# Kernel tuning notes

Hardware: AMD Instinct MI355X
Metric: run time of the kernel (lower is better)

The kernel has to match this reference:

```python
import jax, jax.numpy as jnp
import numpy as np

B = 2
DIMS = ((41, 800, 800), (21, 400, 400), (11, 200, 200), (6, 100, 100))  # (D,H,W)=(z,y,x) per level
VS = ((0.1, 0.1, 0.2), (0.2, 0.2, 0.4), (0.4, 0.4, 0.8), (0.8, 0.8, 1.6))  # (vx,vy,vz)
OFFSET = (0.0, -40.0, -3.0)  # world offset (x,y,z)
BN_EPS = 1e-3

OFFS27 = jnp.array([[z, y, x] for z in (-1, 0, 1) for y in (-1, 0, 1) for x in (-1, 0, 1)], jnp.int32)

# ---------------- numpy-side input construction ----------------

def _np_downsample(coords, out_dims):
    # active output sites of SparseConv3d(k=3, s=2, p=1): in = 2*o - 1 + kd, kd in 0..2
    outs = []
    for kz in range(3):
        for ky in range(3):
            for kx in range(3):
                o = coords[:, 1:] + 1 - np.array([kz, ky, kx])
                ok = (o % 2 == 0).all(1)
                oc = o // 2
                ok &= (oc >= 0).all(1)
                ok &= (oc[:, 0] < out_dims[0]) & (oc[:, 1] < out_dims[1]) & (oc[:, 2] < out_dims[2])
                outs.append(np.concatenate([coords[ok, :1], oc[ok]], 1))
    return np.unique(np.concatenate(outs, 0), axis=0).astype(np.int32)


def _make_coords(rng):
    per_batch = []
    D0, H0, W0 = DIMS[0]
    for b in range(B):
        nc = 120
        centers = np.stack([rng.integers(3, D0 - 4, nc), rng.integers(5, H0 - 6, nc), rng.integers(5, W0 - 6, nc)], 1)
        offs = rng.integers(-3, 4, (nc, 40, 3))
        p = np.clip((centers[:, None, :] + offs).reshape(-1, 3), 0, np.array(DIMS[0]) - 1)
        p = np.unique(p, axis=0)  # sorted lexicographically == sorted by linear key
        per_batch.append(np.concatenate([np.full((len(p), 1), b), p], 1))
    return np.concatenate(per_batch, 0).astype(np.int32)


def setup_inputs():
    rng = np.random.default_rng(0)
    coords0 = _make_coords(rng)
    coords1 = _np_downsample(coords0, DIMS[1])
    coords2 = _np_downsample(coords1, DIMS[2])
    coords3 = _np_downsample(coords2, DIMS[3])
    n = coords0.shape[0]
    c = coords0.astype(np.float64)
    x = OFFSET[0] + (c[:, 3] + 0.5) * VS[0][0] + rng.uniform(-0.04, 0.04, n)
    y = OFFSET[1] + (c[:, 2] + 0.5) * VS[0][1] + rng.uniform(-0.04, 0.04, n)
    z = OFFSET[2] + (c[:, 1] + 0.5) * VS[0][2] + rng.uniform(-0.08, 0.08, n)
    vf = np.stack([x, y, z, rng.uniform(0.0, 1.0, n)], 1).astype(np.float32)

    def conv_w(k, cin, cout):
        return (rng.standard_normal((k, cin, cout)) / np.sqrt(k * cin)).astype(np.float32)

    def bn_p(ch):
        return np.stack([1.0 + 0.05 * rng.standard_normal(ch), 0.05 * rng.standard_normal(ch)], 0).astype(np.float32)

    inp = dict(voxel_features=vf, coords0=coords0, coords1=coords1, coords2=coords2, coords3=coords3,
               w00=conv_w(27, 4, 16), b00=bn_p(16), w01=conv_w(27, 16, 16), b01=bn_p(16),
               wd0=conv_w(27, 16, 32), bd0=bn_p(32),
               w10=conv_w(27, 32, 32), b10=bn_p(32), w11=conv_w(27, 32, 32), b11=bn_p(32),
               wd1=conv_w(27, 32, 64), bd1=bn_p(64),
               w20=conv_w(27, 64, 64), b20=bn_p(64), w21=conv_w(27, 64, 64), b21=bn_p(64), w22=conv_w(27, 64, 64), b22=bn_p(64),
               wd2=conv_w(27, 64, 64), bd2=bn_p(64),
               w30=conv_w(27, 64, 64), b30=bn_p(64), w31=conv_w(27, 64, 64), b31=bn_p(64), w32=conv_w(27, 64, 64), b32=bn_p(64),
               we=(rng.standard_normal((64, 64)) / 8.0).astype(np.float32), be=bn_p(64),
               fc_w=(rng.standard_normal((64, 160)) / np.sqrt(160.0)).astype(np.float32),
               cls_w=(rng.standard_normal((1, 64)) / 8.0).astype(np.float32),
               reg_w=(rng.standard_normal((3, 64)) / 8.0).astype(np.float32))
    return {k: jnp.asarray(v) for k, v in inp.items()}

# ---------------- jax sparse-conv primitives ----------------

def _key(c, dims):
    D, H, W = dims
    return ((c[:, 0] * D + c[:, 1]) * H + c[:, 2]) * W + c[:, 3]


def _gather(nb_b, nb, feats, keys_sorted, dims):
    # nb: (N,27,3) candidate (z,y,x); gather rows of feats via sorted-key lookup, zeros if absent
    D, H, W = dims
    inb = (nb[..., 0] >= 0) & (nb[..., 0] < D) & (nb[..., 1] >= 0) & (nb[..., 1] < H) & (nb[..., 2] >= 0) & (nb[..., 2] < W)
    nbc = jnp.clip(nb, 0, jnp.array(dims, jnp.int32) - 1)
    qk = ((nb_b * D + nbc[..., 0]) * H + nbc[..., 1]) * W + nbc[..., 2]
    pos = jnp.clip(jnp.searchsorted(keys_sorted, qk), 0, keys_sorted.shape[0] - 1)
    found = inb & (keys_sorted[pos] == qk)
    return jnp.where(found[..., None], feats[pos], 0.0)


def _subm(feats, coords, keys, dims, w):
    nb = coords[:, None, 1:] + OFFS27[None]
    g = _gather(coords[:, None, 0], nb, feats, keys, dims)  # (N,27,Cin)
    return jnp.einsum('nkc,kco->no', g, w)


def _stride(feats, in_keys, in_dims, coords_out, w):
    nb = coords_out[:, None, 1:] * 2 + OFFS27[None]  # in = 2*o - 1 + kd
    g = _gather(coords_out[:, None, 0], nb, feats, in_keys, in_dims)
    return jnp.einsum('nkc,kco->no', g, w)


def _bn_relu(x, p):
    # train-mode BatchNorm1d over active voxels (biased var), eps=1e-3
    m = x.mean(0)
    v = jnp.mean((x - m) ** 2, 0)
    return jax.nn.relu((x - m) * jax.lax.rsqrt(v + BN_EPS) * p[0] + p[1])


def _t2p(coords, vs):
    c = coords.astype(jnp.float32)
    x = OFFSET[0] + (c[:, 3] + 0.5) * vs[0]
    y = OFFSET[1] + (c[:, 2] + 0.5) * vs[1]
    z = OFFSET[2] + (c[:, 1] + 0.5) * vs[2]
    return jnp.stack([c[:, 0], x, y, z], 1)


def _nn_interp(unknown, known, feats):
    # three_nn (squared L2, batch-separated, non-differentiable) + three_interpolate
    d2 = jnp.sum((unknown[:, None, 1:] - known[None, :, 1:]) ** 2, -1)
    d2 = d2 + 1e10 * (unknown[:, None, 0] != known[None, :, 0])
    d2 = jax.lax.stop_gradient(d2)
    negd, idx = jax.lax.top_k(-d2, 3)
    w = 1.0 / (-negd + 1e-8)
    w = w / w.sum(1, keepdims=True)
    return jnp.sum(feats[idx] * w[..., None], 1)


def _forward(voxel_features, w00, b00, w01, b01, wd0, bd0, w10, b10, w11, b11, wd1, bd1,
             w20, b20, w21, b21, w22, b22, wd2, bd2, w30, b30, w31, b31, w32, b32,
             we, be, fc_w, cls_w, reg_w, coords0, coords1, coords2, coords3):
    k0, k1 = _key(coords0, DIMS[0]), _key(coords1, DIMS[1])
    k2 = _key(coords2, DIMS[2])
    points_mean = jnp.concatenate([coords0[:, :1].astype(jnp.float32), voxel_features[:, :3]], 1)
    f = _bn_relu(_subm(voxel_features, coords0, k0, DIMS[0], w00), b00)
    f = _bn_relu(_subm(f, coords0, k0, DIMS[0], w01), b01)
    f = _bn_relu(_stride(f, k0, DIMS[0], coords1, wd0), bd0)
    f = _bn_relu(_subm(f, coords1, k1, DIMS[1], w10), b10)
    f = _bn_relu(_subm(f, coords1, k1, DIMS[1], w11), b11)
    p1 = _nn_interp(points_mean, _t2p(coords1, VS[1]), f)
    f = _bn_relu(_stride(f, k1, DIMS[1], coords2, wd1), bd1)
    f = _bn_relu(_subm(f, coords2, k2, DIMS[2], w20), b20)
    f = _bn_relu(_subm(f, coords2, k2, DIMS[2], w21), b21)
    f = _bn_relu(_subm(f, coords2, k2, DIMS[2], w22), b22)
    p2 = _nn_interp(points_mean, _t2p(coords2, VS[2]), f)
    f = _bn_relu(_stride(f, k2, DIMS[2], coords3, wd2), bd2)
    k3 = _key(coords3, DIMS[3])
    f = _bn_relu(_subm(f, coords3, k3, DIMS[3], w30), b30)
    f = _bn_relu(_subm(f, coords3, k3, DIMS[3], w31), b31)
    f = _bn_relu(_subm(f, coords3, k3, DIMS[3], w32), b32)
    p3 = _nn_interp(points_mean, _t2p(coords3, VS[3]), f)
    out = _bn_relu(f @ we, be)  # extra_conv: 1x1x1 SparseConv3d
    D3, H3, W3 = DIMS[3]
    dense = jnp.zeros((B, D3, H3, W3, 64), out.dtype).at[coords3[:, 0], coords3[:, 1], coords3[:, 2], coords3[:, 3]].set(out)
    xd = dense.transpose(0, 4, 1, 2, 3).reshape(B, 64 * D3, H3, W3)  # (N, C*D, H, W)
    pw = jnp.concatenate([p1, p2, p3], 1) @ fc_w.T
    return (xd, points_mean, pw @ cls_w.T, pw @ reg_w.T)


def reference(voxel_features, w00, b00, w01, b01, wd0, bd0, w10, b10, w11, b11, wd1, bd1,
              w20, b20, w21, b21, w22, b22, wd2, bd2, w30, b30, w31, b31, w32, b32,
              we, be, fc_w, cls_w, reg_w, coords0, coords1, coords2, coords3):
    return _forward(voxel_features, w00, b00, w01, b01, wd0, bd0, w10, b10, w11, b11, wd1, bd1,
                    w20, b20, w21, b21, w22, b22, wd2, bd2, w30, b30, w31, b31, w32, b32,
                    we, be, fc_w, cls_w, reg_w, coords0, coords1, coords2, coords3)
```

## Files before the change

kernel.cpp:

```cpp
#include <hip/hip_runtime.h>

#define OFFX 0.0f
#define OFFY -40.0f
#define OFFZ -3.0f
#define BNEPS 1e-3f
#define NCH 128
#define NG 9

typedef _Float16 h2_t __attribute__((ext_vector_type(2)));
__device__ inline h2_t u2h(unsigned u) { union { unsigned u; h2_t h; } x; x.u = u; return x.h; }
__device__ inline unsigned h2u(h2_t h) { union { unsigned u; h2_t h; } x; x.h = h; return x.u; }

__global__ void keys_k(const int* __restrict__ coords, int n, int D, int H, int W,
                       int* __restrict__ keys) {
  int i = blockIdx.x * 256 + threadIdx.x;
  if (i < n) {
    const int* c = coords + (size_t)i * 4;
    keys[i] = ((c[0] * D + c[1]) * H + c[2]) * W + c[3];
  }
}

__global__ void nbr_k(const int* __restrict__ coords, int np, const int* __restrict__ keys, int nk,
                      int D, int H, int W, int scale, int* __restrict__ nbr) {
  int t = blockIdx.x * 256 + threadIdx.x;
  if (t >= np * 27) return;
  int p = t / 27, k = t % 27;
  int kz = k / 9 - 1, ky = (k / 3) % 3 - 1, kx = k % 3 - 1;
  const int* c = coords + (size_t)p * 4;
  int z = c[1] * scale + kz, y = c[2] * scale + ky, x = c[3] * scale + kx;
  int r = -1;
  if (z >= 0 && z < D && y >= 0 && y < H && x >= 0 && x < W) {
    int q = ((c[0] * D + z) * H + y) * W + x;
    int lo = 0, hi = nk;
    while (lo < hi) { int m = (lo + hi) >> 1; if (keys[m] < q) lo = m + 1; else hi = m; }
    if (lo < nk && keys[lo] == q) r = lo;
  }
  nbr[t] = r;
}

struct WPrep { const float* src; unsigned* dst; int cin; int cout; };
struct WP13 { WPrep l[13]; };
__global__ void wprep_k(WP13 a) {
  WPrep w = a.l[blockIdx.y];
  int cp2 = w.cin / 2;
  int tot = 27 * cp2 * w.cout;
  int i = blockIdx.x * 256 + threadIdx.x;
  if (i >= tot) return;
  int o = i % w.cout, rest = i / w.cout;
  int cp = rest % cp2, k = rest / cp2;
  float lo = w.src[((size_t)k * w.cin + 2 * cp) * w.cout + o];
  float hi = w.src[((size_t)k * w.cin + 2 * cp + 1) * w.cout + o];
  h2_t h; h[0] = (_Float16)lo; h[1] = (_Float16)hi;
  w.dst[i] = h2u(h);
}

template<int CIN, int COUT>
__global__ __launch_bounds__(128) void convg_k(const float* __restrict__ feats,
                                               const int* __restrict__ nbr,
                                               const float* __restrict__ w, int n,
                                               float* __restrict__ partial, int gstride) {
  constexpr int TP = 32;
  constexpr int LDP = 36;
  constexpr int CO = COUT / 16;
  __shared__ float G[CIN * LDP];
  int tid = threadIdx.x;
  int pg = tid >> 4, cg = tid & 15;
  int p0 = blockIdx.x * TP;
  int k0 = blockIdx.y * 3;
  float acc[4][CO];
#pragma unroll
  for (int i = 0; i < 4; i++)
#pragma unroll
    for (int j = 0; j < CO; j++) acc[i][j] = 0.f;

  for (int kk = 0; kk < 3; kk++) {
    int k = k0 + kk;
    __syncthreads();
    for (int ch = tid; ch < TP * CIN / 4; ch += 128) {
      int r = ch & (TP - 1), c4 = ch / TP;
      int p = p0 + r;
      int idx = (p < n) ? nbr[(size_t)p * 27 + k] : -1;
      float4 fv = make_float4(0.f, 0.f, 0.f, 0.f);
      if (idx >= 0) fv = *(const float4*)(feats + (size_t)idx * CIN + c4 * 4);
      G[(c4 * 4 + 0) * LDP + r] = fv.x;
      G[(c4 * 4 + 1) * LDP + r] = fv.y;
      G[(c4 * 4 + 2) * LDP + r] = fv.z;
      G[(c4 * 4 + 3) * LDP + r] = fv.w;
    }
    __syncthreads();
    const float* wk = w + (size_t)k * CIN * COUT + cg * CO;
#pragma unroll
    for (int c = 0; c < CIN; c++) {
      float4 g4 = *(const float4*)&G[c * LDP + pg * 4];
      float wv[CO];
      if constexpr (CO == 4)      *(float4*)wv = *(const float4*)(wk + c * COUT);
      else if constexpr (CO == 2) *(float2*)wv = *(const float2*)(wk + c * COUT);
      else                        wv[0] = wk[c * COUT];
      float gp[4] = {g4.x, g4.y, g4.z, g4.w};
#pragma unroll
      for (int i = 0; i < 4; i++)
#pragma unroll
        for (int j = 0; j < CO; j++) acc[i][j] = fmaf(gp[i], wv[j], acc[i][j]);
    }
  }
#pragma unroll
  for (int i = 0; i < 4; i++) {
    int p = p0 + pg * 4 + i;
    if (p < n) {
      float* dst = partial + (size_t)blockIdx.y * gstride + (size_t)p * COUT + cg * CO;
      if constexpr (CO == 4)      *(float4*)dst = *(float4*)acc[i];
      else if constexpr (CO == 2) *(float2*)dst = *(float2*)acc[i];
      else                        dst[0] = acc[i][0];
    }
  }
}

template<int CIN, int COUT>
__global__ __launch_bounds__(128) void convh_k(const unsigned* __restrict__ fh,
                                               const int* __restrict__ nbr,
                                               const unsigned* __restrict__ wh, int n,
                                               void* __restrict__ partial, int gstride,
                                               const float* __restrict__ scsh) {
  constexpr int TP = 32;
  constexpr int LDPH = 36;
  constexpr int CO = COUT / 16;
  constexpr int CP = CIN / 2;
  constexpr bool H2P = (CO >= 2);
  __shared__ unsigned H[CP * LDPH];
  int tid = threadIdx.x;
  int pg = tid >> 4, cg = tid & 15;
  int p0 = blockIdx.x * TP;
  int k0 = blockIdx.y * 3;
  int r = tid & 31;
  int p = p0 + r;
  int sidx[3];
  if (p < n) {
    const int* nb = nbr + (size_t)p * 27 + k0;
    sidx[0] = nb[0]; sidx[1] = nb[1]; sidx[2] = nb[2];
  } else { sidx[0] = sidx[1] = sidx[2] = -1; }

  float acc[4][CO];
#pragma unroll
  for (int i = 0; i < 4; i++)
#pragma unroll
    for (int j = 0; j < CO; j++) acc[i][j] = 0.f;

  if constexpr (CIN >= 32) {
    constexpr int NLD = CIN / 32;
    uint4 pf[NLD];
    {
      int idx = sidx[0];
#pragma unroll
      for (int it = 0; it < NLD; it++) {
        int q = (tid >> 5) + it * 4;
        pf[it] = (idx >= 0) ? *(const uint4*)(fh + (size_t)idx * CP + q * 4)
                            : make_uint4(0, 0, 0, 0);
      }
    }
    for (int kk = 0; kk < 3; kk++) {
      bool ok = sidx[kk] >= 0;
      __syncthreads();
#pragma unroll
      for (int it = 0; it < NLD; it++) {
        int q = (tid >> 5) + it * 4;
        unsigned uu[4] = {pf[it].x, pf[it].y, pf[it].z, pf[it].w};
#pragma unroll
        for (int j = 0; j < 4; j++) {
          int cp = q * 4 + j;
          unsigned outw = 0;
          if (ok) {
            h2_t h = u2h(uu[j]);
            float lo = fmaxf(fmaf((float)h[0], scsh[2 * cp], scsh[CIN + 2 * cp]), 0.f);
            float hi = fmaxf(fmaf((float)h[1], scsh[2 * cp + 1], scsh[CIN + 2 * cp + 1]), 0.f);
            h2_t o; o[0] = (_Float16)lo; o[1] = (_Float16)hi;
            outw = h2u(o);
          }
          H[cp * LDPH + r] = outw;
        }
      }
      if (kk < 2) {
        int idx = sidx[kk + 1];
#pragma unroll
        for (int it = 0; it < NLD; it++) {
          int q = (tid >> 5) + it * 4;
          pf[it] = (idx >= 0) ? *(const uint4*)(fh + (size_t)idx * CP + q * 4)
                              : make_uint4(0, 0, 0, 0);
        }
      }
      __syncthreads();
      const unsigned* wk = wh + (size_t)(k0 + kk) * CP * COUT + cg * CO;
#pragma unroll 8
      for (int cp = 0; cp < CP; cp++) {
        uint4 g4 = *(const uint4*)&H[cp * LDPH + pg * 4];
        unsigned gg[4] = {g4.x, g4.y, g4.z, g4.w};
        unsigned wv[CO];
        if constexpr (CO == 4)      *(uint4*)wv = *(const uint4*)(wk + cp * COUT);
        else if constexpr (CO == 2) *(uint2*)wv = *(const uint2*)(wk + cp * COUT);
        else                        wv[0] = wk[cp * COUT];
#pragma unroll
        for (int i = 0; i < 4; i++)
#pragma unroll
          for (int j = 0; j < CO; j++)
            acc[i][j] = __builtin_amdgcn_fdot2(u2h(gg[i]), u2h(wv[j]), acc[i][j], false);
      }
    }
  } else {
    int q = tid >> 5;
    uint2 pf2;
    {
      int idx = sidx[0];
      pf2 = (idx >= 0) ? *(const uint2*)(fh + (size_t)idx * CP + q * 2) : make_uint2(0, 0);
    }
    for (int kk = 0; kk < 3; kk++) {
      bool ok = sidx[kk] >= 0;
      __syncthreads();
      unsigned uu[2] = {pf2.x, pf2.y};
#pragma unroll
      for (int j = 0; j < 2; j++) {
        int cp = q * 2 + j;
        unsigned outw = 0;
        if (ok) {
          h2_t h = u2h(uu[j]);
          float lo = fmaxf(fmaf((float)h[0], scsh[2 * cp], scsh[CIN + 2 * cp]), 0.f);
          float hi = fmaxf(fmaf((float)h[1], scsh[2 * cp + 1], scsh[CIN + 2 * cp + 1]), 0.f);
          h2_t o; o[0] = (_Float16)lo; o[1] = (_Float16)hi;
          outw = h2u(o);
        }
        H[cp * LDPH + r] = outw;
      }
      if (kk < 2) {
        int idx = sidx[kk + 1];
        pf2 = (idx >= 0) ? *(const uint2*)(fh + (size_t)idx * CP + q * 2) : make_uint2(0, 0);
      }
      __syncthreads();
      const unsigned* wk = wh + (size_t)(k0 + kk) * CP * COUT + cg * CO;
#pragma unroll
      for (int cp = 0; cp < CP; cp++) {
        uint4 g4 = *(const uint4*)&H[cp * LDPH + pg * 4];
        unsigned gg[4] = {g4.x, g4.y, g4.z, g4.w};
        unsigned wv[CO];
        if constexpr (CO == 4)      *(uint4*)wv = *(const uint4*)(wk + cp * COUT);
        else if constexpr (CO == 2) *(uint2*)wv = *(const uint2*)(wk + cp * COUT);
        else                        wv[0] = wk[cp * COUT];
#pragma unroll
        for (int i = 0; i < 4; i++)
#pragma unroll
          for (int j = 0; j < CO; j++)
            acc[i][j] = __builtin_amdgcn_fdot2(u2h(gg[i]), u2h(wv[j]), acc[i][j], false);
      }
    }
  }
#pragma unroll
  for (int i = 0; i < 4; i++) {
    int pp = p0 + pg * 4 + i;
    if (pp < n) {
      if constexpr (H2P) {
        unsigned* dst = (unsigned*)partial + (size_t)blockIdx.y * gstride
                      + (size_t)pp * (COUT / 2) + cg * (CO / 2);
        if constexpr (CO == 4) {
          h2_t a; a[0] = (_Float16)acc[i][0]; a[1] = (_Float16)acc[i][1];
          h2_t b; b[0] = (_Float16)acc[i][2]; b[1] = (_Float16)acc[i][3];
          *(uint2*)dst = make_uint2(h2u(a), h2u(b));
        } else {
          h2_t a; a[0] = (_Float16)acc[i][0]; a[1] = (_Float16)acc[i][1];
          dst[0] = h2u(a);
        }
      } else {
        float* dst = (float*)partial + (size_t)blockIdx.y * gstride
                   + (size_t)pp * COUT + cg * CO;
        dst[0] = acc[i][0];
      }
    }
  }
}

template<bool H2P>
__global__ void bn_k(const void* __restrict__ partial, int G, int gstride, int n, int C,
                     float* __restrict__ pre, unsigned* __restrict__ preh,
                     float* __restrict__ stats, const float* __restrict__ bnp,
                     float* __restrict__ scsh, int* __restrict__ ctr) {
  __shared__ float l1e[256], l2e[256], l1o[256], l2o[256];
  __shared__ int lastf;
  int t = threadIdx.x;
  int total = n * C;
  float s1e = 0.f, s2e = 0.f, s1o = 0.f, s2o = 0.f;
  for (int i2 = (blockIdx.x * 256 + t) * 2; i2 < total; i2 += NCH * 512) {
    float v0 = 0.f, v1 = 0.f;
    if constexpr (H2P) {
      const unsigned* ph = (const unsigned*)partial;
      for (int g = 0; g < G; g++) {
        h2_t h = u2h(ph[(size_t)g * gstride + (i2 >> 1)]);
        v0 += (float)h[0]; v1 += (float)h[1];
      }
    } else {
      const float* pf = (const float*)partial;
      for (int g = 0; g < G; g++) {
        float2 pv = *(const float2*)(pf + (size_t)g * gstride + i2);
        v0 += pv.x; v1 += pv.y;
      }
    }
    if (pre) *(float2*)(pre + i2) = make_float2(v0, v1);
    h2_t h; h[0] = (_Float16)v0; h[1] = (_Float16)v1;
    preh[i2 >> 1] = h2u(h);
    s1e += v0; s2e += v0 * v0; s1o += v1; s2o += v1 * v1;
  }
  l1e[t] = s1e; l2e[t] = s2e; l1o[t] = s1o; l2o[t] = s2o;
  for (int s = 128; s >= C / 2; s >>= 1) {
    __syncthreads();
    if (t < s) {
      l1e[t] += l1e[t + s]; l2e[t] += l2e[t + s];
      l1o[t] += l1o[t + s]; l2o[t] += l2o[t + s];
    }
  }
  __syncthreads();
  if (t < C / 2) {
    stats[((size_t)blockIdx.x * C + 2 * t) * 2]     = l1e[t];
    stats[((size_t)blockIdx.x * C + 2 * t) * 2 + 1] = l2e[t];
    stats[((size_t)blockIdx.x * C + 2 * t + 1) * 2]     = l1o[t];
    stats[((size_t)blockIdx.x * C + 2 * t + 1) * 2 + 1] = l2o[t];
  }
  __threadfence();
  __syncthreads();
  if (t == 0) lastf = (atomicAdd(ctr, 1) == NCH - 1) ? 1 : 0;
  __syncthreads();
  if (lastf) {
    __threadfence();
    int c = t % C, sub = t / C;
    int TPC = 256 / C;
    float a1 = 0.f, a2 = 0.f;
    for (int ch = sub; ch < NCH; ch += TPC) {
      a1 += stats[((size_t)ch * C + c) * 2];
      a2 += stats[((size_t)ch * C + c) * 2 + 1];
    }
    l1e[t] = a1; l2e[t] = a2;
    for (int s = 128; s >= C; s >>= 1) {
      __syncthreads();
      if (t < s) { l1e[t] += l1e[t + s]; l2e[t] += l2e[t + s]; }
    }
    __syncthreads();
    if (t < C) {
      float m = l1e[t] / n;
      float v = l2e[t] / n - m * m;
      float sc = bnp[t] / sqrtf(v + BNEPS);
      scsh[t] = sc;
      scsh[C + t] = bnp[C + t] - m * sc;
    }
  }
}

__global__ void pm_k(const float* __restrict__ vf, const int* __restrict__ c0, int n0,
                     float* __restrict__ pm, float* __restrict__ out1) {
  int i = blockIdx.x * 256 + threadIdx.x;
  if (i >= n0) return;
  float b = (float)c0[(size_t)i * 4];
  float x = vf[(size_t)i * 4], y = vf[(size_t)i * 4 + 1], z = vf[(size_t)i * 4 + 2];
  pm[(size_t)i * 4] = b; pm[(size_t)i * 4 + 1] = x; pm[(size_t)i * 4 + 2] = y; pm[(size_t)i * 4 + 3] = z;
  out1[(size_t)i * 4] = b; out1[(size_t)i * 4 + 1] = x; out1[(size_t)i * 4 + 2] = y; out1[(size_t)i * 4 + 3] = z;
}

__global__ void knnprep_k(const int* __restrict__ coords, int nl, float vx, float vy, float vz,
                          float4* __restrict__ kp4, int* __restrict__ bs) {
  int i = blockIdx.x * 256 + threadIdx.x;
  if (i >= nl) return;
  const int* c = coords + (size_t)i * 4;
  kp4[i] = make_float4(OFFX + (c[3] + 0.5f) * vx,
                       OFFY + (c[2] + 0.5f) * vy,
                       OFFZ + (c[1] + 0.5f) * vz, (float)c[0]);
  if (c[0] == 0 && (i + 1 == nl || coords[(size_t)(i + 1) * 4] == 1)) bs[0] = i + 1;
}

__global__ __launch_bounds__(256) void knn_k(const float4* __restrict__ pm4, int n0,
                                             const float4* __restrict__ kp4, int nl,
                                             const int* __restrict__ bsp,
                                             float* __restrict__ wv, int* __restrict__ iv) {
  __shared__ __align__(16) float4 kp[256];
  __shared__ int bl[4], bh[4];
  int tid = threadIdx.x;
  int wave = tid >> 6, lane = tid & 63;
  int u = blockIdx.x * 4 + wave;
  bool valid = u < n0;
  float4 up = pm4[valid ? u : (n0 - 1)];
  int bs = bsp[0];
  int lo = (up.x == 0.f) ? 0 : bs;
  int hi = (up.x == 0.f) ? bs : nl;
  if (!valid) { lo = 0; hi = 0; }
  if (lane == 0) { bl[wave] = valid ? lo : 0x7fffffff; bh[wave] = valid ? hi : 0; }
  __syncthreads();
  int blo = min(min(bl[0], bl[1]), min(bl[2], bl[3]));
  int bhi = max(max(bh[0], bh[1]), max(bh[2], bh[3]));
  float ux = up.y, uy = up.z, uz = up.w;
  float d0 = 3e38f, d1 = 3e38f, d2 = 3e38f;
  int i0 = -1, i1 = -1, i2 = -1;
#define INS1(DD, GI) { \
    bool l0 = (DD) < d0, l1 = (DD) < d1, l2 = (DD) < d2; \
    i2 = l2 ? (l1 ? i1 : (GI)) : i2; \
    i1 = l1 ? (l0 ? i0 : (GI)) : i1; \
    i0 = l0 ? (GI) : i0; \
    float t1_ = __builtin_amdgcn_fmed3f(d0, d1, (DD)); \
    float t2_ = __builtin_amdgcn_fmed3f(d1, d2, (DD)); \
    d0 = fminf(d0, (DD)); d1 = t1_; d2 = t2_; }
#define DIST(Q) fmaf(ux - (Q).x, ux - (Q).x, fmaf(uy - (Q).y, uy - (Q).y, (uz - (Q).z) * (uz - (Q).z)))
  for (int cb = blo; cb < bhi; cb += 256) {
    int m = bhi - cb; if (m > 256) m = 256;
    __syncthreads();
    if (tid < m) kp[tid] = kp4[cb + tid];
    __syncthreads();
    if (cb + 256 <= lo || cb >= hi) continue;
    if (m == 256 && cb >= lo && cb + 256 <= hi) {
      float4 q0 = kp[lane], q1 = kp[lane + 64], q2 = kp[lane + 128], q3 = kp[lane + 192];
      float a0 = DIST(q0), a1 = DIST(q1), a2 = DIST(q2), a3 = DIST(q3);
      if (__any((a0 < d2) | (a1 < d2) | (a2 < d2) | (a3 < d2))) {
        INS1(a0, cb + lane) INS1(a1, cb + lane + 64)
        INS1(a2, cb + lane + 128) INS1(a3, cb + lane + 192)
      }
    } else {
#pragma unroll
      for (int j = 0; j < 4; j++) {
        int i = lane + 64 * j;
        int e = cb + i;
        if (i < m && e >= lo && e < hi) {
          float4 q = kp[i];
          float dd = DIST(q);
          INS1(dd, e)
        }
      }
    }
  }
#pragma unroll
  for (int off = 1; off < 64; off <<= 1) {
    float e0 = __shfl_xor(d0, off), e1 = __shfl_xor(d1, off), e2 = __shfl_xor(d2, off);
    int j0 = __shfl_xor(i0, off), j1 = __shfl_xor(i1, off), j2 = __shfl_xor(i2, off);
    INS1(e0, j0) INS1(e1, j1) INS1(e2, j2)
  }
#undef DIST
#undef INS1
  if (valid && lane == 0) {
    float w0 = 1.f / (d0 + 1e-8f), w1 = 1.f / (d1 + 1e-8f), w2 = 1.f / (d2 + 1e-8f);
    float s = w0 + w1 + w2;
    wv[(size_t)u * 3] = w0 / s; wv[(size_t)u * 3 + 1] = w1 / s; wv[(size_t)u * 3 + 2] = w2 / s;
    iv[(size_t)u * 3] = i0; iv[(size_t)u * 3 + 1] = i1; iv[(size_t)u * 3 + 2] = i2;
  }
}

__global__ void interp_k(const unsigned* __restrict__ fh, int C, const float* __restrict__ scsh,
                         const float* __restrict__ wv, const int* __restrict__ iv, int n0,
                         float* __restrict__ X, int xoff) {
  int t = blockIdx.x * 256 + threadIdx.x;
  if (t >= n0 * C) return;
  int u = t / C, c = t % C;
  int cp = c >> 1, sel = c & 1;
  int CP = C >> 1;
  float sc = scsh[c], sh = scsh[C + c];
  h2_t h0 = u2h(fh[(size_t)iv[(size_t)u * 3]     * CP + cp]);
  h2_t h1 = u2h(fh[(size_t)iv[(size_t)u * 3 + 1] * CP + cp]);
  h2_t h2v = u2h(fh[(size_t)iv[(size_t)u * 3 + 2] * CP + cp]);
  float a0 = fmaxf(fmaf((float)h0[sel], sc, sh), 0.f);
  float a1 = fmaxf(fmaf((float)h1[sel], sc, sh), 0.f);
  float a2 = fmaxf(fmaf((float)h2v[sel], sc, sh), 0.f);
  X[(size_t)u * 160 + xoff + c] = wv[(size_t)u * 3] * a0 + wv[(size_t)u * 3 + 1] * a1
                                + wv[(size_t)u * 3 + 2] * a2;
}

__global__ __launch_bounds__(256) void conv1x1_k(const unsigned* __restrict__ fh,
                                                 const float* __restrict__ scsh,
                                                 const float* __restrict__ we, int n,
                                                 float* __restrict__ out) {
  __shared__ float rows[256];
  int t = threadIdx.x;
  int p = blockIdx.x * 4 + (t >> 6), c = t & 63;
  float v = 0.f;
  if (p < n) {
    h2_t h = u2h(fh[(size_t)p * 32 + (c >> 1)]);
    v = fmaxf(fmaf((float)h[c & 1], scsh[c], scsh[64 + c]), 0.f);
  }
  rows[t] = v;
  __syncthreads();
  if (p >= n) return;
  const float* fr = rows + (t >> 6) * 64;
  float a = 0.f;
#pragma unroll 16
  for (int ci = 0; ci < 64; ci++) a = fmaf(fr[ci], we[ci * 64 + c], a);
  out[(size_t)p * 64 + c] = a;
}

__global__ void scatter_k(const float* __restrict__ pre, const float* __restrict__ scsh,
                          const int* __restrict__ c3, int n3, float* __restrict__ out0) {
  int t = blockIdx.x * 256 + threadIdx.x;
  if (t >= n3 * 64) return;
  int p = t >> 6, c = t & 63;
  const int* cc = c3 + (size_t)p * 4;
  size_t o = ((((size_t)cc[0] * 64 + c) * 6 + cc[1]) * 100 + cc[2]) * 100 + cc[3];
  out0[o] = fmaxf(fmaf(pre[t], scsh[c], scsh[64 + c]), 0.f);
}

__global__ __launch_bounds__(256) void head_k(const float* __restrict__ X,
                                              const float* __restrict__ fcw,
                                              const float* __restrict__ clsw,
                                              const float* __restrict__ regw,
                                              int n0, float* __restrict__ outc,
                                              float* __restrict__ outr) {
  __shared__ float fl[64 * 161];
  int t = threadIdx.x;
  for (int i = t; i < 64 * 160; i += 256) {
    int r = i / 160, c = i % 160;
    fl[r * 161 + c] = fcw[i];
  }
  __syncthreads();
  int wave = t >> 6, lane = t & 63;
  int u = blockIdx.x * 4 + wave;
  if (u >= n0) return;
  const float* xr = X + (size_t)u * 160;
  const float* wr = fl + (size_t)lane * 161;
  float a = 0.f;
#pragma unroll 8
  for (int i = 0; i < 160; i++) a = fmaf(xr[i], wr[i], a);
  float c = a * clsw[lane];
  float r0 = a * regw[lane], r1 = a * regw[64 + lane], r2 = a * regw[128 + lane];
  for (int off = 32; off; off >>= 1) {
    c  += __shfl_down(c, off);
    r0 += __shfl_down(r0, off);
    r1 += __shfl_down(r1, off);
    r2 += __shfl_down(r2, off);
  }
  if (lane == 0) {
    outc[u] = c;
    outr[(size_t)u * 3] = r0; outr[(size_t)u * 3 + 1] = r1; outr[(size_t)u * 3 + 2] = r2;
  }
}

extern "C" void kernel_launch(void* const* d_in, const int* in_sizes, int n_in,
                              void* d_out, int out_size, void* d_ws, size_t ws_size,
                              hipStream_t stream) {
  const float* vf  = (const float*)d_in[0];
  const int* c0 = (const int*)d_in[1];
  const int* c1 = (const int*)d_in[2];
  const int* c2 = (const int*)d_in[3];
  const int* c3 = (const int*)d_in[4];
  const float* w00 = (const float*)d_in[5];  const float* b00 = (const float*)d_in[6];
  const float* w01 = (const float*)d_in[7];  const float* b01 = (const float*)d_in[8];
  const float* wd0 = (const float*)d_in[9];  const float* bd0 = (const float*)d_in[10];
  const float* w10 = (const float*)d_in[11]; const float* b10 = (const float*)d_in[12];
  const float* w11 = (const float*)d_in[13]; const float* b11 = (const float*)d_in[14];
  const float* wd1 = (const float*)d_in[15]; const float* bd1 = (const float*)d_in[16];
  const float* w20 = (const float*)d_in[17]; const float* b20 = (const float*)d_in[18];
  const float* w21 = (const float*)d_in[19]; const float* b21 = (const float*)d_in[20];
  const float* w22 = (const float*)d_in[21]; const float* b22 = (const float*)d_in[22];
  const float* wd2 = (const float*)d_in[23]; const float* bd2 = (const float*)d_in[24];
  const float* w30 = (const float*)d_in[25]; const float* b30 = (const float*)d_in[26];
  const float* w31 = (const float*)d_in[27]; const float* b31 = (const float*)d_in[28];
  const float* w32 = (const float*)d_in[29]; const float* b32 = (const float*)d_in[30];
  const float* we  = (const float*)d_in[31]; const float* be  = (const float*)d_in[32];
  const float* fcw = (const float*)d_in[33];
  const float* clsw = (const float*)d_in[34];
  const float* regw = (const float*)d_in[35];

  int N0 = in_sizes[1] / 4, N1 = in_sizes[2] / 4, N2 = in_sizes[3] / 4, N3 = in_sizes[4] / 4;
  int maxN = N0; if (N1 > maxN) maxN = N1; if (N2 > maxN) maxN = N2; if (N3 > maxN) maxN = N3;

  auto cdiv = [](int a, int b) { return (a + b - 1) / b; };
  char* p = (char*)d_ws;
  auto alloc = [&](size_t bytes) { char* r = p; p += (bytes + 255) & ~(size_t)255; return r; };

  int* keys0 = (int*)alloc((size_t)N0 * 4);
  int* keys1 = (int*)alloc((size_t)N1 * 4);
  int* keys2 = (int*)alloc((size_t)N2 * 4);
  int* keys3 = (int*)alloc((size_t)N3 * 4);
  int* nbr0  = (int*)alloc((size_t)N0 * 27 * 4);
  int* nbrs1 = (int*)alloc((size_t)N1 * 27 * 4);
  int* nbr1  = (int*)alloc((size_t)N1 * 27 * 4);
  int* nbrs2 = (int*)alloc((size_t)N2 * 27 * 4);
  int* nbr2  = (int*)alloc((size_t)N2 * 27 * 4);
  int* nbrs3 = (int*)alloc((size_t)N3 * 27 * 4);
  int* nbr3  = (int*)alloc((size_t)N3 * 27 * 4);
  float* FA = (float*)alloc((size_t)maxN * 64 * 4);
  float* FB = (float*)alloc((size_t)maxN * 64 * 4);
  float* FC = (float*)alloc((size_t)maxN * 64 * 4);
  unsigned* FAh = (unsigned*)alloc((size_t)maxN * 32 * 4);
  unsigned* FBh = (unsigned*)alloc((size_t)maxN * 32 * 4);
  float* stats = (float*)alloc((size_t)NCH * 64 * 2 * 4);
  float* SC = (float*)alloc((size_t)15 * 128 * 4);
  int* ctrs = (int*)alloc(16 * 4);
  float* wv = (float*)alloc((size_t)N0 * 3 * 4);
  int*   iv = (int*)alloc((size_t)N0 * 3 * 4);
  float* X  = (float*)alloc((size_t)N0 * 160 * 4);
  float* pmb = (float*)alloc((size_t)N0 * 4 * 4);
  float4* kp1 = (float4*)alloc((size_t)N1 * 16);
  float4* kp2 = (float4*)alloc((size_t)N2 * 16);
  float4* kp3 = (float4*)alloc((size_t)N3 * 16);
  int* bsA = (int*)alloc(32);
  unsigned* whbuf = (unsigned*)alloc((size_t)452736 * 4);

  float* out0 = (float*)d_out;
  float* out1 = out0 + 7680000;
  float* outc = out1 + (size_t)N0 * 4;
  float* outr = outc + N0;
  void* partial = out0;

  auto scsh = [&](int L) { return SC + (size_t)L * 128; };

  const float* wsrc[13] = {w01, wd0, w10, w11, wd1, w20, w21, w22, wd2, w30, w31, w32, nullptr};
  int wcin[13]  = {16, 16, 32, 32, 32, 64, 64, 64, 64, 64, 64, 64, 0};
  int wcout[13] = {16, 32, 32, 32, 64, 64, 64, 64, 64, 64, 64, 64, 0};
  unsigned* wdst[13];
  size_t woff = 0;
  WP13 wp{};
  int nw = 12;
  for (int i = 0; i < nw; i++) {
    wdst[i] = whbuf + woff;
    wp.l[i] = WPrep{wsrc[i], wdst[i], wcin[i], wcout[i]};
    woff += (size_t)27 * (wcin[i] / 2) * wcout[i];
  }
  for (int i = nw; i < 13; i++) wp.l[i] = WPrep{w01, wdst[0], 16, 16};

  hipMemsetAsync(ctrs, 0, 16 * 4, stream);
  wprep_k<<<dim3(216, nw), 256, 0, stream>>>(wp);
  keys_k<<<cdiv(N0, 256), 256, 0, stream>>>(c0, N0, 41, 800, 800, keys0);
  keys_k<<<cdiv(N1, 256), 256, 0, stream>>>(c1, N1, 21, 400, 400, keys1);
  keys_k<<<cdiv(N2, 256), 256, 0, stream>>>(c2, N2, 11, 200, 200, keys2);
  keys_k<<<cdiv(N3, 256), 256, 0, stream>>>(c3, N3, 6, 100, 100, keys3);
  nbr_k<<<cdiv(N0 * 27, 256), 256, 0, stream>>>(c0, N0, keys0, N0, 41, 800, 800, 1, nbr0);
  nbr_k<<<cdiv(N1 * 27, 256), 256, 0, stream>>>(c1, N1, keys0, N0, 41, 800, 800, 2, nbrs1);
  nbr_k<<<cdiv(N1 * 27, 256), 256, 0, stream>>>(c1, N1, keys1, N1, 21, 400, 400, 1, nbr1);
  nbr_k<<<cdiv(N2 * 27, 256), 256, 0, stream>>>(c2, N2, keys1, N1, 21, 400, 400, 2, nbrs2);
  nbr_k<<<cdiv(N2 * 27, 256), 256, 0, stream>>>(c2, N2, keys2, N2, 11, 200, 200, 1, nbr2);
  nbr_k<<<cdiv(N3 * 27, 256), 256, 0, stream>>>(c3, N3, keys2, N2, 11, 200, 200, 2, nbrs3);
  nbr_k<<<cdiv(N3 * 27, 256), 256, 0, stream>>>(c3, N3, keys3, N3, 6, 100, 100, 1, nbr3);
  pm_k<<<cdiv(N0, 256), 256, 0, stream>>>(vf, c0, N0, pmb, out1);
  knnprep_k<<<cdiv(N1, 256), 256, 0, stream>>>(c1, N1, 0.2f, 0.2f, 0.4f, kp1, bsA + 0);
  knnprep_k<<<cdiv(N2, 256), 256, 0, stream>>>(c2, N2, 0.4f, 0.4f, 0.8f, kp2, bsA + 1);
  knnprep_k<<<cdiv(N3, 256), 256, 0, stream>>>(c3, N3, 0.8f, 0.8f, 1.6f, kp3, bsA + 2);

  auto convh = [&](const unsigned* fhin, const int* nb, int wi, int n, int cin, int cout,
                   const float* ss) {
    dim3 g(cdiv(n, 32), NG);
    int gs = (cout >= 32) ? n * cout / 2 : n * cout;
    const unsigned* wh = wdst[wi];
    if (cin == 16 && cout == 16)
      convh_k<16, 16><<<g, 128, 0, stream>>>(fhin, nb, wh, n, partial, gs, ss);
    else if (cin == 16 && cout == 32)
      convh_k<16, 32><<<g, 128, 0, stream>>>(fhin, nb, wh, n, partial, gs, ss);
    else if (cin == 32 && cout == 32)
      convh_k<32, 32><<<g, 128, 0, stream>>>(fhin, nb, wh, n, partial, gs, ss);
    else if (cin == 32 && cout == 64)
      convh_k<32, 64><<<g, 128, 0, stream>>>(fhin, nb, wh, n, partial, gs, ss);
    else
      convh_k<64, 64><<<g, 128, 0, stream>>>(fhin, nb, wh, n, partial, gs, ss);
  };
  auto bnp = [&](const float* bnpar, int n, int C, float* pre, unsigned* preh, int L, bool h2p) {
    int gs = h2p ? n * C / 2 : n * C;
    if (h2p)
      bn_k<true><<<NCH, 256, 0, stream>>>(partial, NG, gs, n, C, pre, preh, stats, bnpar,
                                          scsh(L), ctrs + L);
    else
      bn_k<false><<<NCH, 256, 0, stream>>>(partial, NG, gs, n, C, pre, preh, stats, bnpar,
                                           scsh(L), ctrs + L);
  };
  auto knn = [&](const float4* kp4, const int* bsl, int nl, const unsigned* fh, int C, int L,
                 int xoff) {
    knn_k<<<cdiv(N0, 4), 256, 0, stream>>>((const float4*)pmb, N0, kp4, nl, bsl, wv, iv);
    interp_k<<<cdiv(N0 * C, 256), 256, 0, stream>>>(fh, C, scsh(L), wv, iv, N0, X, xoff);
  };

  convg_k<4, 16><<<dim3(cdiv(N0, 32), NG), 128, 0, stream>>>(vf, nbr0, w00, N0,
                                                             (float*)partial, N0 * 16);
  bnp(b00, N0, 16, nullptr, FAh, 0, false);
  convh(FAh, nbr0, 0, N0, 16, 16, scsh(0));   bnp(b01, N0, 16, nullptr, FBh, 1, false);
  convh(FBh, nbrs1, 1, N1, 16, 32, scsh(1));  bnp(bd0, N1, 32, nullptr, FAh, 2, true);
  convh(FAh, nbr1, 2, N1, 32, 32, scsh(2));   bnp(b10, N1, 32, nullptr, FBh, 3, true);
  convh(FBh, nbr1, 3, N1, 32, 32, scsh(3));   bnp(b11, N1, 32, nullptr, FAh, 4, true);
  knn(kp1, bsA + 0, N1, FAh, 32, 4, 0);
  convh(FAh, nbrs2, 4, N2, 32, 64, scsh(4));  bnp(bd1, N2, 64, nullptr, FBh, 5, true);
  convh(FBh, nbr2, 5, N2, 64, 64, scsh(5));   bnp(b20, N2, 64, nullptr, FAh, 6, true);
  convh(FAh, nbr2, 6, N2, 64, 64, scsh(6));   bnp(b21, N2, 64, nullptr, FBh, 7, true);
  convh(FBh, nbr2, 7, N2, 64, 64, scsh(7));   bnp(b22, N2, 64, nullptr, FAh, 8, true);
  knn(kp2, bsA + 1, N2, FAh, 64, 8, 32);
  convh(FAh, nbrs3, 8, N3, 64, 64, scsh(8));  bnp(bd2, N3, 64, nullptr, FBh, 9, true);
  convh(FBh, nbr3, 9, N3, 64, 64, scsh(9));   bnp(b30, N3, 64, nullptr, FAh, 10, true);
  convh(FAh, nbr3, 10, N3, 64, 64, scsh(10)); bnp(b31, N3, 64, nullptr, FBh, 11, true);
  convh(FBh, nbr3, 11, N3, 64, 64, scsh(11)); bnp(b32, N3, 64, nullptr, FAh, 12, true);
  knn(kp3, bsA + 2, N3, FAh, 64, 12, 96);

  conv1x1_k<<<cdiv(N3, 4), 256, 0, stream>>>(FAh, scsh(12), we, N3, FC);
  bn_k<false><<<NCH, 256, 0, stream>>>(FC, 1, 0, N3, 64, FB, FBh, stats, be, scsh(13),
                                       ctrs + 13);
  hipMemsetAsync(d_out, 0, (size_t)7680000 * 4, stream);
  scatter_k<<<cdiv(N3 * 64, 256), 256, 0, stream>>>(FB, scsh(13), c3, N3, out0);
  head_k<<<cdiv(N0, 4), 256, 0, stream>>>(X, fcw, clsw, regw, N0, outc, outr);
}
```

Measured before the change: 866.0 us.

## Fuse prep kernels, share binary search across x-neighbors, fuse KNN with interpolation

Merges the four key-building kernels, point-mean copy and KNN point-prep kernels into one launch. Neighbor lookup now does one binary search per (z,y) row and scans three consecutive keys for the x-neighbors, cutting search work to a third. The KNN kernel broadcasts the top-3 result across the wave and performs the interpolation directly, removing the intermediate weight and index buffers and the separate interp launch. The risks are that the x-scan assumes sorted keys with row-contiguous x, and that KNN lanes now do the extra interpolation work themselves.

Measured after the change: 845.8 us. -2.3%, faster.

```diff
diff --git a/kernel.cpp b/kernel.cpp
--- a/kernel.cpp
+++ b/kernel.cpp
@@ -11,31 +11,75 @@
 __device__ inline h2_t u2h(unsigned u) { union { unsigned u; h2_t h; } x; x.u = u; return x.h; }
 __device__ inline unsigned h2u(h2_t h) { union { unsigned u; h2_t h; } x; x.h = h; return x.u; }
 
-__global__ void keys_k(const int* __restrict__ coords, int n, int D, int H, int W,
-                       int* __restrict__ keys) {
+struct PrepA {
+  const int *c0, *c1, *c2, *c3;
+  int n0, n1, n2, n3;
+  int *k0, *k1, *k2, *k3;
+  float4 *kp1, *kp2, *kp3;
+  int* bs;
+  const float* vf; float* pmb; float* out1;
+};
+__global__ void prep_k(PrepA a) {
   int i = blockIdx.x * 256 + threadIdx.x;
-  if (i < n) {
-    const int* c = coords + (size_t)i * 4;
-    keys[i] = ((c[0] * D + c[1]) * H + c[2]) * W + c[3];
+  if (i < a.n0) {
+    const int* c = a.c0 + (size_t)i * 4;
+    a.k0[i] = ((c[0] * 41 + c[1]) * 800 + c[2]) * 800 + c[3];
+    float b = (float)c[0];
+    float x = a.vf[(size_t)i * 4], y = a.vf[(size_t)i * 4 + 1], z = a.vf[(size_t)i * 4 + 2];
+    a.pmb[(size_t)i * 4] = b; a.pmb[(size_t)i * 4 + 1] = x;
+    a.pmb[(size_t)i * 4 + 2] = y; a.pmb[(size_t)i * 4 + 3] = z;
+    a.out1[(size_t)i * 4] = b; a.out1[(size_t)i * 4 + 1] = x;
+    a.out1[(size_t)i * 4 + 2] = y; a.out1[(size_t)i * 4 + 3] = z;
+  }
+  if (i < a.n1) {
+    const int* c = a.c1 + (size_t)i * 4;
+    a.k1[i] = ((c[0] * 21 + c[1]) * 400 + c[2]) * 400 + c[3];
+    a.kp1[i] = make_float4(OFFX + (c[3] + 0.5f) * 0.2f, OFFY + (c[2] + 0.5f) * 0.2f,
+                           OFFZ + (c[1] + 0.5f) * 0.4f, (float)c[0]);
+    if (c[0] == 0 && (i + 1 == a.n1 || a.c1[(size_t)(i + 1) * 4] == 1)) a.bs[0] = i + 1;
+  }
+  if (i < a.n2) {
+    const int* c = a.c2 + (size_t)i * 4;
+    a.k2[i] = ((c[0] * 11 + c[1]) * 200 + c[2]) * 200 + c[3];
+    a.kp2[i] = make_float4(OFFX + (c[3] + 0.5f) * 0.4f, OFFY + (c[2] + 0.5f) * 0.4f,
+                           OFFZ + (c[1] + 0.5f) * 0.8f, (float)c[0]);
+    if (c[0] == 0 && (i + 1 == a.n2 || a.c2[(size_t)(i + 1) * 4] == 1)) a.bs[1] = i + 1;
+  }
+  if (i < a.n3) {
+    const int* c = a.c3 + (size_t)i * 4;
+    a.k3[i] = ((c[0] * 6 + c[1]) * 100 + c[2]) * 100 + c[3];
+    a.kp3[i] = make_float4(OFFX + (c[3] + 0.5f) * 0.8f, OFFY + (c[2] + 0.5f) * 0.8f,
+                           OFFZ + (c[1] + 0.5f) * 1.6f, (float)c[0]);
+    if (c[0] == 0 && (i + 1 == a.n3 || a.c3[(size_t)(i + 1) * 4] == 1)) a.bs[2] = i + 1;
   }
 }
 
 __global__ void nbr_k(const int* __restrict__ coords, int np, const int* __restrict__ keys, int nk,
                       int D, int H, int W, int scale, int* __restrict__ nbr) {
   int t = blockIdx.x * 256 + threadIdx.x;
-  if (t >= np * 27) return;
-  int p = t / 27, k = t % 27;
-  int kz = k / 9 - 1, ky = (k / 3) % 3 - 1, kx = k % 3 - 1;
+  if (t >= np * 9) return;
+  int p = t / 9, j = t % 9;
+  int kz = j / 3 - 1, ky = j % 3 - 1;
   const int* c = coords + (size_t)p * 4;
-  int z = c[1] * scale + kz, y = c[2] * scale + ky, x = c[3] * scale + kx;
-  int r = -1;
-  if (z >= 0 && z < D && y >= 0 && y < H && x >= 0 && x < W) {
-    int q = ((c[0] * D + z) * H + y) * W + x;
+  int z = c[1] * scale + kz, y = c[2] * scale + ky;
+  int xb = c[3] * scale - 1;
+  int r[3] = {-1, -1, -1};
+  if (z >= 0 && z < D && y >= 0 && y < H) {
+    int qb = ((c[0] * D + z) * H + y) * W + xb;
     int lo = 0, hi = nk;
-    while (lo < hi) { int m = (lo + hi) >> 1; if (keys[m] < q) lo = m + 1; else hi = m; }
-    if (lo < nk && keys[lo] == q) r = lo;
-  }
-  nbr[t] = r;
+    while (lo < hi) { int m = (lo + hi) >> 1; if (keys[m] < qb) lo = m + 1; else hi = m; }
+#pragma unroll
+    for (int dx = 0; dx < 3; dx++) {
+      int q = qb + dx;
+      int xq = xb + dx;
+      if (lo < nk && keys[lo] == q) {
+        if (xq >= 0 && xq < W) r[dx] = lo;
+        lo++;
+      }
+    }
+  }
+  int* dst = nbr + (size_t)p * 27 + j * 3;
+  dst[0] = r[0]; dst[1] = r[1]; dst[2] = r[2];
 }
 
 struct WPrep { const float* src; unsigned* dst; int cin; int cout; };
@@ -348,31 +392,12 @@
   }
 }
 
-__global__ void pm_k(const float* __restrict__ vf, const int* __restrict__ c0, int n0,
-                     float* __restrict__ pm, float* __restrict__ out1) {
-  int i = blockIdx.x * 256 + threadIdx.x;
-  if (i >= n0) return;
-  float b = (float)c0[(size_t)i * 4];
-  float x = vf[(size_t)i * 4], y = vf[(size_t)i * 4 + 1], z = vf[(size_t)i * 4 + 2];
-  pm[(size_t)i * 4] = b; pm[(size_t)i * 4 + 1] = x; pm[(size_t)i * 4 + 2] = y; pm[(size_t)i * 4 + 3] = z;
-  out1[(size_t)i * 4] = b; out1[(size_t)i * 4 + 1] = x; out1[(size_t)i * 4 + 2] = y; out1[(size_t)i * 4 + 3] = z;
-}
-
-__global__ void knnprep_k(const int* __restrict__ coords, int nl, float vx, float vy, float vz,
-                          float4* __restrict__ kp4, int* __restrict__ bs) {
-  int i = blockIdx.x * 256 + threadIdx.x;
-  if (i >= nl) return;
-  const int* c = coords + (size_t)i * 4;
-  kp4[i] = make_float4(OFFX + (c[3] + 0.5f) * vx,
-                       OFFY + (c[2] + 0.5f) * vy,
-                       OFFZ + (c[1] + 0.5f) * vz, (float)c[0]);
-  if (c[0] == 0 && (i + 1 == nl || coords[(size_t)(i + 1) * 4] == 1)) bs[0] = i + 1;
-}
-
-__global__ __launch_bounds__(256) void knn_k(const float4* __restrict__ pm4, int n0,
-                                             const float4* __restrict__ kp4, int nl,
-                                             const int* __restrict__ bsp,
-                                             float* __restrict__ wv, int* __restrict__ iv) {
+__global__ __launch_bounds__(256) void knni_k(const float4* __restrict__ pm4, int n0,
+                                              const float4* __restrict__ kp4, int nl,
+                                              const int* __restrict__ bsp,
+                                              const unsigned* __restrict__ fh, int C,
+                                              const float* __restrict__ scsh,
+                                              float* __restrict__ X, int xoff) {
   __shared__ __align__(16) float4 kp[256];
   __shared__ int bl[4], bh[4];
   int tid = threadIdx.x;
@@ -434,31 +459,29 @@
   }
 #undef DIST
 #undef INS1
-  if (valid && lane == 0) {
+  i0 = __shfl(i0, 0); i1 = __shfl(i1, 0); i2 = __shfl(i2, 0);
+  d0 = __shfl(d0, 0); d1 = __shfl(d1, 0); d2 = __shfl(d2, 0);
+  if (valid && i0 >= 0) {
     float w0 = 1.f / (d0 + 1e-8f), w1 = 1.f / (d1 + 1e-8f), w2 = 1.f / (d2 + 1e-8f);
     float s = w0 + w1 + w2;
-    wv[(size_t)u * 3] = w0 / s; wv[(size_t)u * 3 + 1] = w1 / s; wv[(size_t)u * 3 + 2] = w2 / s;
-    iv[(size_t)u * 3] = i0; iv[(size_t)u * 3 + 1] = i1; iv[(size_t)u * 3 + 2] = i2;
-  }
-}
-
-__global__ void interp_k(const unsigned* __restrict__ fh, int C, const float* __restrict__ scsh,
-                         const float* __restrict__ wv, const int* __restrict__ iv, int n0,
-                         float* __restrict__ X, int xoff) {
-  int t = blockIdx.x * 256 + threadIdx.x;
-  if (t >= n0 * C) return;
-  int u = t / C, c = t % C;
-  int cp = c >> 1, sel = c & 1;
-  int CP = C >> 1;
-  float sc = scsh[c], sh = scsh[C + c];
-  h2_t h0 = u2h(fh[(size_t)iv[(size_t)u * 3]     * CP + cp]);
-  h2_t h1 = u2h(fh[(size_t)iv[(size_t)u * 3 + 1] * CP + cp]);
-  h2_t h2v = u2h(fh[(size_t)iv[(size_t)u * 3 + 2] * CP + cp]);
-  float a0 = fmaxf(fmaf((float)h0[sel], sc, sh), 0.f);
-  float a1 = fmaxf(fmaf((float)h1[sel], sc, sh), 0.f);
-  float a2 = fmaxf(fmaf((float)h2v[sel], sc, sh), 0.f);
-  X[(size_t)u * 160 + xoff + c] = wv[(size_t)u * 3] * a0 + wv[(size_t)u * 3 + 1] * a1
-                                + wv[(size_t)u * 3 + 2] * a2;
+    w0 /= s; w1 /= s; w2 /= s;
+    int CP = C >> 1;
+    for (int cp = lane; cp < CP; cp += 64) {
+      h2_t h0 = u2h(fh[(size_t)i0 * CP + cp]);
+      h2_t h1 = u2h(fh[(size_t)i1 * CP + cp]);
+      h2_t h2v = u2h(fh[(size_t)i2 * CP + cp]);
+      int ce = 2 * cp, co = 2 * cp + 1;
+      float se = scsh[ce], he = scsh[C + ce];
+      float so = scsh[co], ho = scsh[C + co];
+      float ae = w0 * fmaxf(fmaf((float)h0[0], se, he), 0.f)
+               + w1 * fmaxf(fmaf((float)h1[0], se, he), 0.f)
+               + w2 * fmaxf(fmaf((float)h2v[0], se, he), 0.f);
+      float ao = w0 * fmaxf(fmaf((float)h0[1], so, ho), 0.f)
+               + w1 * fmaxf(fmaf((float)h1[1], so, ho), 0.f)
+               + w2 * fmaxf(fmaf((float)h2v[1], so, ho), 0.f);
+      *(float2*)(X + (size_t)u * 160 + xoff + ce) = make_float2(ae, ao);
+    }
+  }
 }
 
 __global__ __launch_bounds__(256) void conv1x1_k(const unsigned* __restrict__ fh,
@@ -572,7 +595,6 @@
   int* nbr2  = (int*)alloc((size_t)N2 * 27 * 4);
   int* nbrs3 = (int*)alloc((size_t)N3 * 27 * 4);
   int* nbr3  = (int*)alloc((size_t)N3 * 27 * 4);
-  float* FA = (float*)alloc((size_t)maxN * 64 * 4);
   float* FB = (float*)alloc((size_t)maxN * 64 * 4);
   float* FC = (float*)alloc((size_t)maxN * 64 * 4);
   unsigned* FAh = (unsigned*)alloc((size_t)maxN * 32 * 4);
@@ -580,8 +602,6 @@
   float* stats = (float*)alloc((size_t)NCH * 64 * 2 * 4);
   float* SC = (float*)alloc((size_t)15 * 128 * 4);
   int* ctrs = (int*)alloc(16 * 4);
-  float* wv = (float*)alloc((size_t)N0 * 3 * 4);
-  int*   iv = (int*)alloc((size_t)N0 * 3 * 4);
   float* X  = (float*)alloc((size_t)N0 * 160 * 4);
   float* pmb = (float*)alloc((size_t)N0 * 4 * 4);
   float4* kp1 = (float4*)alloc((size_t)N1 * 16);
@@ -614,21 +634,20 @@
 
   hipMemsetAsync(ctrs, 0, 16 * 4, stream);
   wprep_k<<<dim3(216, nw), 256, 0, stream>>>(wp);
-  keys_k<<<cdiv(N0, 256), 256, 0, stream>>>(c0, N0, 41, 800, 800, keys0);
-  keys_k<<<cdiv(N1, 256), 256, 0, stream>>>(c1, N1, 21, 400, 400, keys1);
-  keys_k<<<cdiv(N2, 256), 256, 0, stream>>>(c2, N2, 11, 200, 200, keys2);
-  keys_k<<<cdiv(N3, 256), 256, 0, stream>>>(c3, N3, 6, 100, 100, keys3);
-  nbr_k<<<cdiv(N0 * 27, 256), 256, 0, stream>>>(c0, N0, keys0, N0, 41, 800, 800, 1, nbr0);
-  nbr_k<<<cdiv(N1 * 27, 256), 256, 0, stream>>>(c1, N1, keys0, N0, 41, 800, 800, 2, nbrs1);
-  nbr_k<<<cdiv(N1 * 27, 256), 256, 0, stream>>>(c1, N1, keys1, N1, 21, 400, 400, 1, nbr1);
-  nbr_k<<<cdiv(N2 * 27, 256), 256, 0, stream>>>(c2, N2, keys1, N1, 21, 400, 400, 2, nbrs2);
-  nbr_k<<<cdiv(N2 * 27, 256), 256, 0, stream>>>(c2, N2, keys2, N2, 11, 200, 200, 1, nbr2);
-  nbr_k<<<cdiv(N3 * 27, 256), 256, 0, stream>>>(c3, N3, keys2, N2, 11, 200, 200, 2, nbrs3);
-  nbr_k<<<cdiv(N3 * 27, 256), 256, 0, stream>>>(c3, N3, keys3, N3, 6, 100, 100, 1, nbr3);
-  pm_k<<<cdiv(N0, 256), 256, 0, stream>>>(vf, c0, N0, pmb, out1);
-  knnprep_k<<<cdiv(N1, 256), 256, 0, stream>>>(c1, N1, 0.2f, 0.2f, 0.4f, kp1, bsA + 0);
-  knnprep_k<<<cdiv(N2, 256), 256, 0, stream>>>(c2, N2, 0.4f, 0.4f, 0.8f, kp2, bsA + 1);
-  knnprep_k<<<cdiv(N3, 256), 256, 0, stream>>>(c3, N3, 0.8f, 0.8f, 1.6f, kp3, bsA + 2);
+  PrepA pa;
+  pa.c0 = c0; pa.c1 = c1; pa.c2 = c2; pa.c3 = c3;
+  pa.n0 = N0; pa.n1 = N1; pa.n2 = N2; pa.n3 = N3;
+  pa.k0 = keys0; pa.k1 = keys1; pa.k2 = keys2; pa.k3 = keys3;
+  pa.kp1 = kp1; pa.kp2 = kp2; pa.kp3 = kp3;
+  pa.bs = bsA; pa.vf = vf; pa.pmb = pmb; pa.out1 = out1;
+  prep_k<<<cdiv(maxN, 256), 256, 0, stream>>>(pa);
+  nbr_k<<<cdiv(N0 * 9, 256), 256, 0, stream>>>(c0, N0, keys0, N0, 41, 800, 800, 1, nbr0);
+  nbr_k<<<cdiv(N1 * 9, 256), 256, 0, stream>>>(c1, N1, keys0, N0, 41, 800, 800, 2, nbrs1);
+  nbr_k<<<cdiv(N1 * 9, 256), 256, 0, stream>>>(c1, N1, keys1, N1, 21, 400, 400, 1, nbr1);
+  nbr_k<<<cdiv(N2 * 9, 256), 256, 0, stream>>>(c2, N2, keys1, N1, 21, 400, 400, 2, nbrs2);
+  nbr_k<<<cdiv(N2 * 9, 256), 256, 0, stream>>>(c2, N2, keys2, N2, 11, 200, 200, 1, nbr2);
+  nbr_k<<<cdiv(N3 * 9, 256), 256, 0, stream>>>(c3, N3, keys2, N2, 11, 200, 200, 2, nbrs3);
+  nbr_k<<<cdiv(N3 * 9, 256), 256, 0, stream>>>(c3, N3, keys3, N3, 6, 100, 100, 1, nbr3);
 
   auto convh = [&](const unsigned* fhin, const int* nb, int wi, int n, int cin, int cout,
                    const float* ss) {
@@ -657,8 +676,8 @@
   };
   auto knn = [&](const float4* kp4, const int* bsl, int nl, const unsigned* fh, int C, int L,
                  int xoff) {
-    knn_k<<<cdiv(N0, 4), 256, 0, stream>>>((const float4*)pmb, N0, kp4, nl, bsl, wv, iv);
-    interp_k<<<cdiv(N0 * C, 256), 256, 0, stream>>>(fh, C, scsh(L), wv, iv, N0, X, xoff);
+    knni_k<<<cdiv(N0, 4), 256, 0, stream>>>((const float4*)pmb, N0, kp4, nl, bsl,
+                                            fh, C, scsh(L), X, xoff);
   };
 
   convg_k<4, 16><<<dim3(cdiv(N0, 32), NG), 128, 0, stream>>>(vf, nbr0, w00, N0,
```
